# Optimization experiments

Measured on AMD Instinct MI355X. Metric: run time of the kernel, lower is better.

The kernel has to match this reference:

```python
import jax, jax.numpy as jnp
import numpy as np

N_NODES = 100000
N_EDGES = 1600000
NUM_PROP = 5
CAT_PROP = 3
INPUT_DIM = 128
HIDDEN = 128
NUM_REL = 2


def setup_inputs() -> dict:
    key = jax.random.key(0)
    ks = jax.random.split(key, 20)
    s = 0.05
    inp = {
        "x": jax.random.normal(ks[0], (N_NODES, NUM_PROP + CAT_PROP), jnp.float32),
        "edge_index": jax.random.randint(ks[1], (2, N_EDGES), 0, N_NODES, jnp.int64 if jax.config.jax_enable_x64 else jnp.int32),
        "edge_type": jax.random.randint(ks[2], (N_EDGES,), 0, NUM_REL, jnp.int32),
        # numeric / categorical encoders -> input_dim/2 each
        "W_num": jax.random.normal(ks[3], (NUM_PROP, INPUT_DIM // 2), jnp.float32) * s,
        "b_num": jnp.zeros((INPUT_DIM // 2,), jnp.float32),
        "W_cat": jax.random.normal(ks[4], (CAT_PROP, INPUT_DIM // 2), jnp.float32) * s,
        "b_cat": jnp.zeros((INPUT_DIM // 2,), jnp.float32),
        # input projection + PReLU
        "W_in": jax.random.normal(ks[5], (INPUT_DIM, HIDDEN), jnp.float32) * s,
        "b_in": jnp.zeros((HIDDEN,), jnp.float32),
        "prelu_a": jnp.full((HIDDEN,), 0.25, jnp.float32),
        # RGCN layer 1
        "W_rel1": jax.random.normal(ks[6], (NUM_REL, HIDDEN, HIDDEN), jnp.float32) * s,
        "W_root1": jax.random.normal(ks[7], (HIDDEN, HIDDEN), jnp.float32) * s,
        "b_rgcn1": jnp.zeros((HIDDEN,), jnp.float32),
        # RGCN layer 2
        "W_rel2": jax.random.normal(ks[8], (NUM_REL, HIDDEN, HIDDEN), jnp.float32) * s,
        "W_root2": jax.random.normal(ks[9], (HIDDEN, HIDDEN), jnp.float32) * s,
        "b_rgcn2": jnp.zeros((HIDDEN,), jnp.float32),
        # classifier (single Linear)
        "W_cls": jax.random.normal(ks[10], (HIDDEN, HIDDEN), jnp.float32) * s,
        "b_cls": jnp.zeros((HIDDEN,), jnp.float32),
    }
    return inp


def _leaky_relu(x, slope=0.01):
    return jnp.where(x >= 0, x, slope * x)


def _prelu(x, a):
    return jnp.where(x >= 0, x, a * x)


def _rgcn_conv(x, edge_index, edge_type, W_rel, W_root, bias):
    # PyG RGCNConv: out[i] = x[i] @ W_root + bias + sum_r mean_{j in N_r(i)} x[j] @ W_r
    # Aggregate-then-transform (linearity) to avoid per-edge (E, d) @ W products.
    src, dst = edge_index[0], edge_index[1]
    n = x.shape[0]
    x_src = x[src]  # (E, d) gather
    out = x @ W_root + bias
    for r in range(W_rel.shape[0]):
        w = (edge_type == r).astype(x.dtype)  # (E,)
        agg = jax.ops.segment_sum(x_src * w[:, None], dst, num_segments=n)  # (N, d)
        deg = jax.ops.segment_sum(w, dst, num_segments=n)  # (N,)
        out = out + (agg / jnp.clip(deg, 1.0)[:, None]) @ W_rel[r]
    return out


def reference(x, edge_index, edge_type, W_num, b_num, W_cat, b_cat, W_in, b_in,
              prelu_a, W_rel1, W_root1, b_rgcn1, W_rel2, W_root2, b_rgcn2,
              W_cls, b_cls):
    num_prop = x[:, :NUM_PROP]
    cat_prop = x[:, NUM_PROP:NUM_PROP + CAT_PROP]
    n = _leaky_relu(num_prop @ W_num + b_num)
    c = _leaky_relu(cat_prop @ W_cat + b_cat)
    h = jnp.concatenate([n, c], axis=1)
    h = _prelu(h @ W_in + b_in, prelu_a)
    h = _rgcn_conv(h, edge_index, edge_type, W_rel1, W_root1, b_rgcn1)
    # dropout is identity in eval mode
    h = _rgcn_conv(h, edge_index, edge_type, W_rel2, W_root2, b_rgcn2)
    return h @ W_cls + b_cls
```

## Files before the change

kernel.cpp:

```cpp
#include <hip/hip_runtime.h>
#include <cstdint>


typedef short bf16x8 __attribute__((ext_vector_type(8)));
typedef float f32x4  __attribute__((ext_vector_type(4)));

__device__ __forceinline__ unsigned short f2bf(float f) {
    unsigned int u = __builtin_bit_cast(unsigned int, f);
    u += 0x7fff + ((u >> 16) & 1);
    return (unsigned short)(u >> 16);
}
__device__ __forceinline__ float bf2f(unsigned short h) {
    unsigned int u = ((unsigned int)h) << 16;
    return __builtin_bit_cast(float, u);
}
__device__ __forceinline__ float lo16f(unsigned int u) {
    return __builtin_bit_cast(float, u << 16);
}
__device__ __forceinline__ float hi16f(unsigned int u) {
    return __builtin_bit_cast(float, u & 0xffff0000u);
}

__device__ __forceinline__ void gload_lds16(const void* g, void* l) {
    __builtin_amdgcn_global_load_lds(
        (const __attribute__((address_space(1))) void*)g,
        (__attribute__((address_space(3))) void*)l, 16, 0, 0);
}

__global__ __launch_bounds__(256) void k_pre(
    const float* __restrict__ x,
    const float* __restrict__ Wnum, const float* __restrict__ bnum,
    const float* __restrict__ Wcat, const float* __restrict__ bcat,
    unsigned short* __restrict__ hi, unsigned short* __restrict__ lo, int N,
    const int* __restrict__ ei, const int* __restrict__ et,
    int* __restrict__ cntmat, int E, int NBLK, int NBINS)
{
    __shared__ int hist[1024];
    const int t = threadIdx.x;
    const int blk = blockIdx.x;

    if (blk < NBLK) {
        for (int i = t; i < NBINS; i += 256) hist[i] = 0;
        __syncthreads();
        #pragma unroll
        for (int j = 0; j < 8; ++j) {
            int e = blk * 2048 + j * 256 + t;
            if (e < E) {
                int seg = et[e] * N + ei[E + e];
                atomicAdd(&hist[seg >> 8], 1);
            }
        }
        __syncthreads();
        for (int i = t; i < NBINS; i += 256)
            cntmat[(size_t)i * NBLK + blk] = hist[i];
    }

    int gid = blk * 256 + t;
    if (gid < N * 32) {
        int n = gid >> 5, kq = (gid & 31) << 2;
        const float* xr = x + n * 8;
        float vv[4];
        #pragma unroll
        for (int q = 0; q < 4; ++q) {
            int k = kq + q;
            float acc;
            if (k < 64) {
                acc = bnum[k];
                #pragma unroll
                for (int p = 0; p < 5; ++p) acc += xr[p] * Wnum[p * 64 + k];
            } else {
                int kk = k - 64;
                acc = bcat[kk];
                #pragma unroll
                for (int p = 0; p < 3; ++p) acc += xr[5 + p] * Wcat[p * 64 + kk];
            }
            vv[q] = acc >= 0.f ? acc : 0.01f * acc;
        }
        ushort4 h, l;
        h.x = f2bf(vv[0]); l.x = f2bf(vv[0] - bf2f(h.x));
        h.y = f2bf(vv[1]); l.y = f2bf(vv[1] - bf2f(h.y));
        h.z = f2bf(vv[2]); l.z = f2bf(vv[2] - bf2f(h.z));
        h.w = f2bf(vv[3]); l.w = f2bf(vv[3] - bf2f(h.w));
        ((ushort4*)hi)[gid] = h;
        ((ushort4*)lo)[gid] = l;
    }
}

struct WArgs {
    const float* W[8];
    unsigned short* hi[8];
    unsigned short* lo[8];
};
__global__ __launch_bounds__(256) void k_wsplit(WArgs a)
{
    int part = blockIdx.y;
    int idx = blockIdx.x * 256 + threadIdx.x;
    int n = idx >> 7, k = idx & 127;
    float v = a.W[part][(size_t)k * 128 + n];
    unsigned short h = f2bf(v);
    a.hi[part][(size_t)n * 128 + k] = h;
    a.lo[part][(size_t)n * 128 + k] = f2bf(v - bf2f(h));
}

__global__ __launch_bounds__(256) void k_scan1(
    const int* __restrict__ src, int* __restrict__ dst,
    int* __restrict__ bsum, int n)
{
    __shared__ int s[256];
    int t = threadIdx.x;
    int i = blockIdx.x * 256 + t;
    int v = (i < n) ? src[i] : 0;
    s[t] = v;
    __syncthreads();
    #pragma unroll
    for (int d = 1; d < 256; d <<= 1) {
        int add = (t >= d) ? s[t - d] : 0;
        __syncthreads();
        s[t] += add;
        __syncthreads();
    }
    if (i < n) dst[i] = s[t] - v;
    if (t == 255) bsum[blockIdx.x] = s[255];
}

__global__ __launch_bounds__(1024) void k_scan2(int* __restrict__ bsum, int nb)
{
    __shared__ int s[1024];
    int t = threadIdx.x;
    int carry = 0;
    for (int base = 0; base < nb; base += 1024) {
        int i = base + t;
        int v = (i < nb) ? bsum[i] : 0;
        s[t] = v;
        __syncthreads();
        #pragma unroll
        for (int d = 1; d < 1024; d <<= 1) {
            int add = (t >= d) ? s[t - d] : 0;
            __syncthreads();
            s[t] += add;
            __syncthreads();
        }
        if (i < nb) bsum[i] = carry + s[t] - v;
        carry += s[1023];
        __syncthreads();
    }
}

__global__ __launch_bounds__(256) void k_scan3(
    int* __restrict__ dst, const int* __restrict__ bsum, int n)
{
    int i = blockIdx.x * 256 + threadIdx.x;
    if (i < n) dst[i] += bsum[blockIdx.x];
}

__global__ __launch_bounds__(256) void k_binscatter(
    const int* __restrict__ ei, const int* __restrict__ et,
    const int* __restrict__ cntscan, int* __restrict__ ebuf,
    int E, int N, int NBLK, int NBINS)
{
    __shared__ int base[1024];
    const int t = threadIdx.x;
    const int blk = blockIdx.x;
    for (int i = t; i < NBINS; i += 256)
        base[i] = cntscan[(size_t)i * NBLK + blk];
    __syncthreads();
    #pragma unroll
    for (int j = 0; j < 8; ++j) {
        int e = blk * 2048 + j * 256 + t;
        if (e < E) {
            unsigned src = (unsigned)ei[e];
            int seg = et[e] * N + ei[E + e];
            int pos = atomicAdd(&base[seg >> 8], 1);
            ebuf[pos] = (int)(((unsigned)(seg & 255) << 24) | src);
        }
    }
}

__global__ __launch_bounds__(256) void k_bincsr(
    const int* __restrict__ cntscan, const int* __restrict__ ebuf,
    int* __restrict__ deg, int* __restrict__ off, int* __restrict__ esrc,
    int E, int nseg, int NBLK, int NBINS)
{
    __shared__ int cnt[256];
    __shared__ int pfx[256];
    __shared__ int cur[256];
    const int b = blockIdx.x;
    const int t = threadIdx.x;
    const int est = cntscan[(size_t)b * NBLK];
    const int een = (b + 1 < NBINS) ? cntscan[(size_t)(b + 1) * NBLK] : E;
    cnt[t] = 0;
    __syncthreads();
    for (int e = est + t; e < een; e += 256)
        atomicAdd(&cnt[((unsigned)ebuf[e]) >> 24], 1);
    __syncthreads();
    int v = cnt[t];
    pfx[t] = v;
    __syncthreads();
    #pragma unroll
    for (int d = 1; d < 256; d <<= 1) {
        int add = (t >= d) ? pfx[t - d] : 0;
        __syncthreads();
        pfx[t] += add;
        __syncthreads();
    }
    int o = est + pfx[t] - v;
    int seg = b * 256 + t;
    if (seg < nseg) { deg[seg] = v; off[seg] = o; }
    cur[t] = o;
    __syncthreads();
    for (int e = est + t; e < een; e += 256) {
        unsigned u = (unsigned)ebuf[e];
        int p = atomicAdd(&cur[u >> 24], 1);
        esrc[p] = (int)(u & 0xffffffu);
    }
}

__global__ __launch_bounds__(256) void k_gather(
    const unsigned short* __restrict__ h_hi,
    const int* __restrict__ esrc,
    const int* __restrict__ off, const int* __restrict__ deg,
    unsigned short* __restrict__ a_hi, int nseg)
{
    int i = blockIdx.x * 8 + (threadIdx.x >> 5);
    if (i >= nseg) return;
    int l32 = threadIdx.x & 31;
    int q = l32 >> 4;
    int l16 = l32 & 15;
    int cnt = deg[i], st = off[i];
    const uint4* hp = (const uint4*)h_hi;
    float a0 = 0.f, a1 = 0.f, a2 = 0.f, a3 = 0.f;
    float a4 = 0.f, a5 = 0.f, a6 = 0.f, a7 = 0.f;
    int e = q;
    for (; e + 6 < cnt; e += 8) {
        int i0 = esrc[st + e + 0];
        int i1 = esrc[st + e + 2];
        int i2 = esrc[st + e + 4];
        int i3 = esrc[st + e + 6];
        uint4 u0 = hp[(size_t)i0 * 16 + l16];
        uint4 u1 = hp[(size_t)i1 * 16 + l16];
        uint4 u2 = hp[(size_t)i2 * 16 + l16];
        uint4 u3 = hp[(size_t)i3 * 16 + l16];
        a0 += lo16f(u0.x); a1 += hi16f(u0.x); a2 += lo16f(u0.y); a3 += hi16f(u0.y);
        a4 += lo16f(u0.z); a5 += hi16f(u0.z); a6 += lo16f(u0.w); a7 += hi16f(u0.w);
        a0 += lo16f(u1.x); a1 += hi16f(u1.x); a2 += lo16f(u1.y); a3 += hi16f(u1.y);
        a4 += lo16f(u1.z); a5 += hi16f(u1.z); a6 += lo16f(u1.w); a7 += hi16f(u1.w);
        a0 += lo16f(u2.x); a1 += hi16f(u2.x); a2 += lo16f(u2.y); a3 += hi16f(u2.y);
        a4 += lo16f(u2.z); a5 += hi16f(u2.z); a6 += lo16f(u2.w); a7 += hi16f(u2.w);
        a0 += lo16f(u3.x); a1 += hi16f(u3.x); a2 += lo16f(u3.y); a3 += hi16f(u3.y);
        a4 += lo16f(u3.z); a5 += hi16f(u3.z); a6 += lo16f(u3.w); a7 += hi16f(u3.w);
    }
    for (; e < cnt; e += 2) {
        uint4 u = hp[(size_t)esrc[st + e] * 16 + l16];
        a0 += lo16f(u.x); a1 += hi16f(u.x); a2 += lo16f(u.y); a3 += hi16f(u.y);
        a4 += lo16f(u.z); a5 += hi16f(u.z); a6 += lo16f(u.w); a7 += hi16f(u.w);
    }
    a0 += __shfl_xor(a0, 16, 64);
    a1 += __shfl_xor(a1, 16, 64);
    a2 += __shfl_xor(a2, 16, 64);
    a3 += __shfl_xor(a3, 16, 64);
    a4 += __shfl_xor(a4, 16, 64);
    a5 += __shfl_xor(a5, 16, 64);
    a6 += __shfl_xor(a6, 16, 64);
    a7 += __shfl_xor(a7, 16, 64);
    if (q == 0) {
        float inv = 1.0f / (float)(cnt > 1 ? cnt : 1);
        uint4 o;
        o.x = (unsigned int)f2bf(a0 * inv) | ((unsigned int)f2bf(a1 * inv) << 16);
        o.y = (unsigned int)f2bf(a2 * inv) | ((unsigned int)f2bf(a3 * inv) << 16);
        o.z = (unsigned int)f2bf(a4 * inv) | ((unsigned int)f2bf(a5 * inv) << 16);
        o.w = (unsigned int)f2bf(a6 * inv) | ((unsigned int)f2bf(a7 * inv) << 16);
        ((uint4*)a_hi)[(size_t)i * 16 + l16] = o;
    }
}

struct GArgs {
    const unsigned short* A_hi[3];
    const unsigned short* A_lo[3];
    const unsigned short* B_hi[3];
    const unsigned short* B_lo[3];
    int alo[3];
    int blo[3];
    const float* bias;
    const float* prelu;
    float* Cf;
    unsigned short* C_hi;
    unsigned short* C_lo;
    int M;
    int P;
};

__global__ __launch_bounds__(256) void k_mgemm(GArgs g)
{
    __shared__ unsigned short lds[2][32 * 512];
    const int t = threadIdx.x;
    const int w = t >> 6, lane = t & 63;
    const int laneL = lane & 15, laneH = lane >> 4;
    const int wi = w >> 1, wj = w & 1;
    const int m0 = blockIdx.x * 128;
    const int Mm1 = g.M - 1;
    const int S = g.P * 4;

    f32x4 acc[4][4];
    #pragma unroll
    for (int a = 0; a < 4; ++a)
        #pragma unroll
        for (int b = 0; b < 4; ++b)
            acc[a][b] = (f32x4){0.f, 0.f, 0.f, 0.f};

    auto stage = [&](int s, unsigned short* buf) {
        int p = s >> 2, koff = (s & 3) * 32;
        const unsigned short* tp[4];
        tp[0] = g.A_hi[p];
        tp[1] = g.alo[p] ? g.A_lo[p] : nullptr;
        tp[2] = g.B_hi[p];
        tp[3] = g.blo[p] ? g.B_lo[p] : nullptr;
        #pragma unroll
        for (int c = 0; c < 8; ++c) {
            int chunk = w + c * 4;
            int slot = chunk >> 3, j = chunk & 7;
            const unsigned short* plane = tp[slot];
            if (!plane) continue;
            int rc = j * 16 + laneL;
            int row = (slot < 2) ? (m0 + rc <= Mm1 ? m0 + rc : Mm1) : rc;
            const unsigned short* gp = plane + (size_t)row * 128 + koff + laneH * 8;
            gload_lds16(gp, &buf[(slot * 8 + j) * 512]);
        }
    };

    stage(0, lds[0]);
    for (int s = 0; s < S; ++s) {
        unsigned short* cur = lds[s & 1];
        unsigned short* nxt = lds[(s & 1) ^ 1];
        __syncthreads();
        if (s + 1 < S) stage(s + 1, nxt);
        int p = s >> 2;
        const bool hasAlo = g.alo[p] != 0;
        const bool hasBlo = g.blo[p] != 0;
        const bf16x8* fr = (const bf16x8*)cur;
        bf16x8 ah[4], al[4], bh[4], bl[4];
        #pragma unroll
        for (int mi = 0; mi < 4; ++mi)
            ah[mi] = fr[(0 + wi * 4 + mi) * 64 + lane];
        if (hasAlo) {
            #pragma unroll
            for (int mi = 0; mi < 4; ++mi)
                al[mi] = fr[(8 + wi * 4 + mi) * 64 + lane];
        }
        #pragma unroll
        for (int nj = 0; nj < 4; ++nj)
            bh[nj] = fr[(16 + wj * 4 + nj) * 64 + lane];
        if (hasBlo) {
            #pragma unroll
            for (int nj = 0; nj < 4; ++nj)
                bl[nj] = fr[(24 + wj * 4 + nj) * 64 + lane];
        }
        #pragma unroll
        for (int mi = 0; mi < 4; ++mi)
            #pragma unroll
            for (int nj = 0; nj < 4; ++nj) {
                acc[mi][nj] = __builtin_amdgcn_mfma_f32_16x16x32_bf16(
                    ah[mi], bh[nj], acc[mi][nj], 0, 0, 0);
                if (hasBlo)
                    acc[mi][nj] = __builtin_amdgcn_mfma_f32_16x16x32_bf16(
                        ah[mi], bl[nj], acc[mi][nj], 0, 0, 0);
                if (hasAlo)
                    acc[mi][nj] = __builtin_amdgcn_mfma_f32_16x16x32_bf16(
                        al[mi], bh[nj], acc[mi][nj], 0, 0, 0);
            }
    }

    const bool hasPrelu = (g.prelu != nullptr);
    float bv[4], av[4];
    #pragma unroll
    for (int nj = 0; nj < 4; ++nj) {
        int col = wj * 64 + nj * 16 + laneL;
        bv[nj] = g.bias[col];
        av[nj] = hasPrelu ? g.prelu[col] : 0.f;
    }

    if (g.Cf) {
        float* lf = (float*)&lds[0][0];
        __syncthreads();
        #pragma unroll
        for (int nj = 0; nj < 4; ++nj) {
            int col = wj * 64 + nj * 16 + laneL;
            #pragma unroll
            for (int mi = 0; mi < 4; ++mi)
                #pragma unroll
                for (int r = 0; r < 4; ++r) {
                    int row = wi * 64 + mi * 16 + laneH * 4 + r;
                    float v = acc[mi][nj][r] + bv[nj];
                    lf[row * 128 + col] = v;
                }
        }
        __syncthreads();
        const uint4* lsrc = (const uint4*)lf;
        #pragma unroll
        for (int it = 0; it < 16; ++it) {
            int idx = it * 256 + t;
            int row = idx >> 5, c = idx & 31;
            int m = m0 + row;
            if (m < g.M)
                ((uint4*)(g.Cf + (size_t)m * 128))[c] = lsrc[idx];
        }
    } else {
        unsigned short* lp = &lds[0][0];
        __syncthreads();
        #pragma unroll
        for (int nj = 0; nj < 4; ++nj) {
            int col = wj * 64 + nj * 16 + laneL;
            #pragma unroll
            for (int mi = 0; mi < 4; ++mi)
                #pragma unroll
                for (int r = 0; r < 4; ++r) {
                    int row = wi * 64 + mi * 16 + laneH * 4 + r;
                    float v = acc[mi][nj][r] + bv[nj];
                    if (hasPrelu) v = v >= 0.f ? v : av[nj] * v;
                    lp[row * 128 + col] = f2bf(v);
                }
        }
        __syncthreads();
        {
            const uint4* lsrc = (const uint4*)lp;
            #pragma unroll
            for (int it = 0; it < 8; ++it) {
                int idx = it * 256 + t;
                int row = idx >> 4, c = idx & 15;
                int m = m0 + row;
                if (m < g.M)
                    ((uint4*)(g.C_hi + (size_t)m * 128))[c] = lsrc[idx];
            }
        }
        __syncthreads();
        #pragma unroll
        for (int nj = 0; nj < 4; ++nj) {
            int col = wj * 64 + nj * 16 + laneL;
            #pragma unroll
            for (int mi = 0; mi < 4; ++mi)
                #pragma unroll
                for (int r = 0; r < 4; ++r) {
                    int row = wi * 64 + mi * 16 + laneH * 4 + r;
                    float v = acc[mi][nj][r] + bv[nj];
                    if (hasPrelu) v = v >= 0.f ? v : av[nj] * v;
                    unsigned short h = f2bf(v);
                    lp[row * 128 + col] = f2bf(v - bf2f(h));
                }
        }
        __syncthreads();
        {
            const uint4* lsrc = (const uint4*)lp;
            #pragma unroll
            for (int it = 0; it < 8; ++it) {
                int idx = it * 256 + t;
                int row = idx >> 4, c = idx & 15;
                int m = m0 + row;
                if (m < g.M)
                    ((uint4*)(g.C_lo + (size_t)m * 128))[c] = lsrc[idx];
            }
        }
    }
}

extern "C" void kernel_launch(void* const* d_in, const int* in_sizes, int n_in,
                              void* d_out, int out_size, void* d_ws, size_t ws_size,
                              hipStream_t stream) {
    const float* x      = (const float*)d_in[0];
    const int*   ei     = (const int*)d_in[1];
    const int*   et     = (const int*)d_in[2];
    const float* Wnum   = (const float*)d_in[3];
    const float* bnum   = (const float*)d_in[4];
    const float* Wcat   = (const float*)d_in[5];
    const float* bcat   = (const float*)d_in[6];
    const float* Win    = (const float*)d_in[7];
    const float* bin    = (const float*)d_in[8];
    const float* pa     = (const float*)d_in[9];
    const float* Wrel1  = (const float*)d_in[10];
    const float* Wroot1 = (const float*)d_in[11];
    const float* brg1   = (const float*)d_in[12];
    const float* Wrel2  = (const float*)d_in[13];
    const float* Wroot2 = (const float*)d_in[14];
    const float* brg2   = (const float*)d_in[15];
    const float* Wcls   = (const float*)d_in[16];
    const float* bcls   = (const float*)d_in[17];
    float* out = (float*)d_out;

    const int N = in_sizes[0] / 8;
    const int E = in_sizes[1] / 2;
    const int nseg = 2 * N;
    const size_t NH = (size_t)N * 128;

    const int NBLK  = (E + 2047) / 2048;
    const int NBINS = (nseg + 255) / 256;
    const long long L = (long long)NBINS * NBLK;

    char* w = (char*)d_ws;
    unsigned short* h0_hi = (unsigned short*)w;  w += NH * 2;
    unsigned short* h0_lo = (unsigned short*)w;  w += NH * 2;
    unsigned short* agg_hi = (unsigned short*)w; w += 2 * NH * 2;
    int* deg     = (int*)w;  w += (size_t)nseg * 4;
    int* off     = (int*)w;  w += (size_t)nseg * 4;
    int* cntmat  = (int*)w;  w += (size_t)L * 4;
    int* cntscan = (int*)w;  w += (size_t)L * 4;
    int* esrc    = (int*)w;  w += (size_t)E * 4;
    int* bsum    = (int*)w;  w += 4096 * 4;
    unsigned short* wplanes = (unsigned short*)w;  w += 8 * 2 * 16384 * 2;

    unsigned short* hp_hi = agg_hi;
    unsigned short* hp_lo = agg_hi + NH;
    unsigned short* h1_hi = (unsigned short*)d_out;
    unsigned short* h1_lo = h1_hi + NH;
    unsigned short* h2_hi = h0_hi;
    unsigned short* h2_lo = h0_lo;
    int* ebuf = (int*)d_out;

    unsigned short* whi[8];
    unsigned short* wlo[8];
    for (int i = 0; i < 8; ++i) {
        whi[i] = wplanes + (size_t)i * 2 * 16384;
        wlo[i] = whi[i] + 16384;
    }

    {
        WArgs a;
        a.W[0] = Win;   a.W[1] = Wroot1; a.W[2] = Wrel1; a.W[3] = Wrel1 + 16384;
        a.W[4] = Wroot2; a.W[5] = Wrel2; a.W[6] = Wrel2 + 16384; a.W[7] = Wcls;
        for (int i = 0; i < 8; ++i) { a.hi[i] = whi[i]; a.lo[i] = wlo[i]; }
        k_wsplit<<<dim3(64, 8), 256, 0, stream>>>(a);
    }

    const int gm = (N + 127) / 128;
    const int gg = (nseg + 7) / 8;

    {
        int gA = (N * 32 + 255) / 256;
        int gpre = gA > NBLK ? gA : NBLK;
        k_pre<<<gpre, 256, 0, stream>>>(x, Wnum, bnum, Wcat, bcat,
                                        hp_hi, hp_lo, N, ei, et,
                                        cntmat, E, NBLK, NBINS);
    }

    const int nb1 = (int)((L + 255) / 256);
    k_scan1<<<nb1, 256, 0, stream>>>(cntmat, cntscan, bsum, (int)L);
    k_scan2<<<1, 1024, 0, stream>>>(bsum, nb1);
    k_scan3<<<nb1, 256, 0, stream>>>(cntscan, bsum, (int)L);

    k_binscatter<<<NBLK, 256, 0, stream>>>(ei, et, cntscan, ebuf, E, N, NBLK, NBINS);
    k_bincsr<<<NBINS, 256, 0, stream>>>(cntscan, ebuf, deg, off, esrc, E, nseg, NBLK, NBINS);

    {
        GArgs g = {};
        g.A_hi[0] = hp_hi; g.A_lo[0] = hp_lo; g.alo[0] = 1; g.blo[0] = 1;
        g.B_hi[0] = whi[0]; g.B_lo[0] = wlo[0];
        g.bias = bin; g.prelu = pa;
        g.Cf = nullptr; g.C_hi = h0_hi; g.C_lo = h0_lo;
        g.M = N; g.P = 1;
        k_mgemm<<<gm, 256, 0, stream>>>(g);
    }
    k_gather<<<gg, 256, 0, stream>>>(h0_hi, esrc, off, deg, agg_hi, nseg);
    {
        GArgs g = {};
        g.A_hi[0] = h0_hi;       g.A_lo[0] = h0_lo;  g.alo[0] = 1; g.blo[0] = 1;
        g.A_hi[1] = agg_hi;      g.alo[1] = 0;       g.blo[1] = 0;
        g.A_hi[2] = agg_hi + NH; g.alo[2] = 0;       g.blo[2] = 0;
        g.B_hi[0] = whi[1]; g.B_lo[0] = wlo[1];
        g.B_hi[1] = whi[2]; g.B_lo[1] = wlo[2];
        g.B_hi[2] = whi[3]; g.B_lo[2] = wlo[3];
        g.bias = brg1; g.prelu = nullptr;
        g.Cf = nullptr; g.C_hi = h1_hi; g.C_lo = h1_lo;
        g.M = N; g.P = 3;
        k_mgemm<<<gm, 256, 0, stream>>>(g);
    }
    k_gather<<<gg, 256, 0, stream>>>(h1_hi, esrc, off, deg, agg_hi, nseg);
    {
        GArgs g = {};
        g.A_hi[0] = h1_hi;       g.A_lo[0] = h1_lo;  g.alo[0] = 1; g.blo[0] = 1;
        g.A_hi[1] = agg_hi;      g.alo[1] = 0;       g.blo[1] = 0;
        g.A_hi[2] = agg_hi + NH; g.alo[2] = 0;       g.blo[2] = 0;
        g.B_hi[0] = whi[4]; g.B_lo[0] = wlo[4];
        g.B_hi[1] = whi[5]; g.B_lo[1] = wlo[5];
        g.B_hi[2] = whi[6]; g.B_lo[2] = wlo[6];
        g.bias = brg2; g.prelu = nullptr;
        g.Cf = nullptr; g.C_hi = h2_hi; g.C_lo = h2_lo;
        g.M = N; g.P = 3;
        k_mgemm<<<gm, 256, 0, stream>>>(g);
    }
    {
        GArgs g = {};
        g.A_hi[0] = h2_hi; g.A_lo[0] = h2_lo; g.alo[0] = 1; g.blo[0] = 1;
        g.B_hi[0] = whi[7]; g.B_lo[0] = wlo[7];
        g.bias = bcls; g.prelu = nullptr;
        g.Cf = out; g.C_hi = nullptr; g.C_lo = nullptr;
        g.M = N; g.P = 1;
        k_mgemm<<<gm, 256, 0, stream>>>(g);
    }
}
```

Before: 536.5 us.

## Split histogram from node encoder and transpose count matrix for coalesced access

Separates the edge histogram from the node-feature encoder into its own kernel and writes per-block counts block-major, so stores are coalesced. Explicit tiled transposes convert to bin-major for the scan and back to block-major for the scatter. The encoder now computes 8 outputs per thread with 16-byte stores. The cost is two extra kernel launches and extra traffic over the count matrix, which is about 1.2M entries.

```diff
diff --git a/kernel.cpp b/kernel.cpp
--- a/kernel.cpp
+++ b/kernel.cpp
@@ -31,58 +31,86 @@
     const float* __restrict__ x,
     const float* __restrict__ Wnum, const float* __restrict__ bnum,
     const float* __restrict__ Wcat, const float* __restrict__ bcat,
-    unsigned short* __restrict__ hi, unsigned short* __restrict__ lo, int N,
+    unsigned short* __restrict__ hi, unsigned short* __restrict__ lo, int N)
+{
+    int gid = blockIdx.x * 256 + threadIdx.x;
+    if (gid >= N * 16) return;
+    int n = gid >> 4, k8 = (gid & 15) << 3;
+    const float* xr = x + n * 8;
+    float xv[8];
+    #pragma unroll
+    for (int p = 0; p < 8; ++p) xv[p] = xr[p];
+    unsigned hw[4], lw[4];
+    #pragma unroll
+    for (int q = 0; q < 8; ++q) {
+        int k = k8 + q;
+        float acc;
+        if (k < 64) {
+            acc = bnum[k];
+            #pragma unroll
+            for (int p = 0; p < 5; ++p) acc += xv[p] * Wnum[p * 64 + k];
+        } else {
+            int kk = k - 64;
+            acc = bcat[kk];
+            #pragma unroll
+            for (int p = 0; p < 3; ++p) acc += xv[5 + p] * Wcat[p * 64 + kk];
+        }
+        float v = acc >= 0.f ? acc : 0.01f * acc;
+        unsigned short h = f2bf(v);
+        unsigned short l = f2bf(v - bf2f(h));
+        if (q & 1) {
+            hw[q >> 1] |= (unsigned)h << 16;
+            lw[q >> 1] |= (unsigned)l << 16;
+        } else {
+            hw[q >> 1] = h;
+            lw[q >> 1] = l;
+        }
+    }
+    uint4 ho, loo;
+    ho.x = hw[0]; ho.y = hw[1]; ho.z = hw[2]; ho.w = hw[3];
+    loo.x = lw[0]; loo.y = lw[1]; loo.z = lw[2]; loo.w = lw[3];
+    ((uint4*)hi)[gid] = ho;
+    ((uint4*)lo)[gid] = loo;
+}
+
+__global__ __launch_bounds__(256) void k_hist(
     const int* __restrict__ ei, const int* __restrict__ et,
-    int* __restrict__ cntmat, int E, int NBLK, int NBINS)
+    int* __restrict__ cntmatT, int E, int N, int NBINS)
 {
     __shared__ int hist[1024];
-    const int t = threadIdx.x;
-    const int blk = blockIdx.x;
-
-    if (blk < NBLK) {
-        for (int i = t; i < NBINS; i += 256) hist[i] = 0;
-        __syncthreads();
-        #pragma unroll
-        for (int j = 0; j < 8; ++j) {
-            int e = blk * 2048 + j * 256 + t;
-            if (e < E) {
-                int seg = et[e] * N + ei[E + e];
-                atomicAdd(&hist[seg >> 8], 1);
-            }
-        }
-        __syncthreads();
-        for (int i = t; i < NBINS; i += 256)
-            cntmat[(size_t)i * NBLK + blk] = hist[i];
-    }
-
-    int gid = blk * 256 + t;
-    if (gid < N * 32) {
-        int n = gid >> 5, kq = (gid & 31) << 2;
-        const float* xr = x + n * 8;
-        float vv[4];
-        #pragma unroll
-        for (int q = 0; q < 4; ++q) {
-            int k = kq + q;
-            float acc;
-            if (k < 64) {
-                acc = bnum[k];
-                #pragma unroll
-                for (int p = 0; p < 5; ++p) acc += xr[p] * Wnum[p * 64 + k];
-            } else {
-                int kk = k - 64;
-                acc = bcat[kk];
-                #pragma unroll
-                for (int p = 0; p < 3; ++p) acc += xr[5 + p] * Wcat[p * 64 + kk];
-            }
-            vv[q] = acc >= 0.f ? acc : 0.01f * acc;
-        }
-        ushort4 h, l;
-        h.x = f2bf(vv[0]); l.x = f2bf(vv[0] - bf2f(h.x));
-        h.y = f2bf(vv[1]); l.y = f2bf(vv[1] - bf2f(h.y));
-        h.z = f2bf(vv[2]); l.z = f2bf(vv[2] - bf2f(h.z));
-        h.w = f2bf(vv[3]); l.w = f2bf(vv[3] - bf2f(h.w));
-        ((ushort4*)hi)[gid] = h;
-        ((ushort4*)lo)[gid] = l;
+    const int t = threadIdx.x, blk = blockIdx.x;
+    for (int i = t; i < NBINS; i += 256) hist[i] = 0;
+    __syncthreads();
+    #pragma unroll
+    for (int j = 0; j < 8; ++j) {
+        int e = blk * 2048 + j * 256 + t;
+        if (e < E) atomicAdd(&hist[(et[e] * N + ei[E + e]) >> 8], 1);
+    }
+    __syncthreads();
+    for (int i = t; i < NBINS; i += 256)
+        cntmatT[(size_t)blk * NBINS + i] = hist[i];
+}
+
+__global__ __launch_bounds__(256) void k_transpose(
+    const int* __restrict__ src, int* __restrict__ dst, int R, int C)
+{
+    __shared__ int tile[32][33];
+    int ctiles = (C + 31) >> 5;
+    int bx = blockIdx.x % ctiles;
+    int by = blockIdx.x / ctiles;
+    int tc = threadIdx.x & 31, tr = threadIdx.x >> 5;
+    int c0 = bx * 32, r0 = by * 32;
+    #pragma unroll
+    for (int i = 0; i < 32; i += 8) {
+        int r = r0 + tr + i, c = c0 + tc;
+        if (r < R && c < C) tile[tr + i][tc] = src[(size_t)r * C + c];
+    }
+    __syncthreads();
+    #pragma unroll
+    for (int i = 0; i < 32; i += 8) {
+        int r = r0 + tc;
+        int c = c0 + tr + i;
+        if (r < R && c < C) dst[(size_t)c * R + r] = tile[tc][tr + i];
     }
 }
 
@@ -155,14 +183,14 @@
 
 __global__ __launch_bounds__(256) void k_binscatter(
     const int* __restrict__ ei, const int* __restrict__ et,
-    const int* __restrict__ cntscan, int* __restrict__ ebuf,
-    int E, int N, int NBLK, int NBINS)
+    const int* __restrict__ cntscanT, int* __restrict__ ebuf,
+    int E, int N, int NBINS)
 {
     __shared__ int base[1024];
     const int t = threadIdx.x;
     const int blk = blockIdx.x;
     for (int i = t; i < NBINS; i += 256)
-        base[i] = cntscan[(size_t)i * NBLK + blk];
+        base[i] = cntscanT[(size_t)blk * NBINS + i];
     __syncthreads();
     #pragma unroll
     for (int j = 0; j < 8; ++j) {
@@ -497,12 +525,14 @@
     unsigned short* h0_hi = (unsigned short*)w;  w += NH * 2;
     unsigned short* h0_lo = (unsigned short*)w;  w += NH * 2;
     unsigned short* agg_hi = (unsigned short*)w; w += 2 * NH * 2;
-    int* deg     = (int*)w;  w += (size_t)nseg * 4;
-    int* off     = (int*)w;  w += (size_t)nseg * 4;
-    int* cntmat  = (int*)w;  w += (size_t)L * 4;
-    int* cntscan = (int*)w;  w += (size_t)L * 4;
-    int* esrc    = (int*)w;  w += (size_t)E * 4;
-    int* bsum    = (int*)w;  w += 4096 * 4;
+    int* deg      = (int*)w;  w += (size_t)nseg * 4;
+    int* off      = (int*)w;  w += (size_t)nseg * 4;
+    int* cntmatT  = (int*)w;  w += (size_t)L * 4;
+    int* cntmat   = (int*)w;  w += (size_t)L * 4;
+    int* cntscan  = (int*)w;  w += (size_t)L * 4;
+    int* cntscanT = (int*)w;  w += (size_t)L * 4;
+    int* esrc     = (int*)w;  w += (size_t)E * 4;
+    int* bsum     = (int*)w;  w += 4096 * 4;
     unsigned short* wplanes = (unsigned short*)w;  w += 8 * 2 * 16384 * 2;
 
     unsigned short* hp_hi = agg_hi;
@@ -531,20 +561,22 @@
     const int gm = (N + 127) / 128;
     const int gg = (nseg + 7) / 8;
 
-    {
-        int gA = (N * 32 + 255) / 256;
-        int gpre = gA > NBLK ? gA : NBLK;
-        k_pre<<<gpre, 256, 0, stream>>>(x, Wnum, bnum, Wcat, bcat,
-                                        hp_hi, hp_lo, N, ei, et,
-                                        cntmat, E, NBLK, NBINS);
-    }
+    k_pre<<<(N * 16 + 255) / 256, 256, 0, stream>>>(
+        x, Wnum, bnum, Wcat, bcat, hp_hi, hp_lo, N);
+
+    k_hist<<<NBLK, 256, 0, stream>>>(ei, et, cntmatT, E, N, NBINS);
+
+    const int rt = (NBLK + 31) / 32, ct = (NBINS + 31) / 32;
+    k_transpose<<<rt * ct, 256, 0, stream>>>(cntmatT, cntmat, NBLK, NBINS);
 
     const int nb1 = (int)((L + 255) / 256);
     k_scan1<<<nb1, 256, 0, stream>>>(cntmat, cntscan, bsum, (int)L);
     k_scan2<<<1, 1024, 0, stream>>>(bsum, nb1);
     k_scan3<<<nb1, 256, 0, stream>>>(cntscan, bsum, (int)L);
 
-    k_binscatter<<<NBLK, 256, 0, stream>>>(ei, et, cntscan, ebuf, E, N, NBLK, NBINS);
+    k_transpose<<<ct * rt, 256, 0, stream>>>(cntscan, cntscanT, NBINS, NBLK);
+
+    k_binscatter<<<NBLK, 256, 0, stream>>>(ei, et, cntscanT, ebuf, E, N, NBINS);
     k_bincsr<<<NBINS, 256, 0, stream>>>(cntscan, ebuf, deg, off, esrc, E, nseg, NBLK, NBINS);
 
     {
```

After: 583.7 us. +8.8%, slower.
